# Performance work log

Hardware: AMD Instinct MI355X
Metric: run time of the kernel (lower is better)

## Reference

```python
import jax, jax.numpy as jnp
import numpy as np

# Static configuration (uniform ragged layout: every sequence has the same lengths)
B = 8          # number of sequences
QLEN = 256     # new query tokens per sequence
D = 1024       # embedding_dim
H = 16         # num_attention_heads
HD = D // H    # head dim = 64
FFN = 4096     # ffn_embedding_dim
PAGE = 16      # KV-cache page size
KV_TOTAL = 4096            # total KV length per sequence (prefix + new)
P = KV_TOTAL // PAGE       # pages per sequence = 256
NEW_PAGES = QLEN // PAGE   # pages occupied by the new tokens = 16
NUM_PAGES = B * P          # 2048
PREFIX = KV_TOTAL - QLEN   # cached prefix length per sequence
SCALE = HD ** -0.5
LN_EPS = 1e-5


def layer_norm(x, g, b):
    mu = jnp.mean(x, axis=-1, keepdims=True)
    var = jnp.mean(jnp.square(x - mu), axis=-1, keepdims=True)
    return (x - mu) * jax.lax.rsqrt(var + LN_EPS) * g + b


def setup_inputs() -> dict:
    key = jax.random.key(0)
    ks = jax.random.split(key, 12)
    s = 0.02
    inp = {
        "x": jax.random.normal(ks[0], (B * QLEN, D), jnp.float32),
        "pagetable": jax.random.normal(ks[1], (NUM_PAGES, 2, PAGE, H, HD), jnp.float32) * 0.5,
        "Wq": jax.random.normal(ks[2], (D, D), jnp.float32) * s,
        "bq": jnp.zeros((D,), jnp.float32),
        "Wk": jax.random.normal(ks[3], (D, D), jnp.float32) * s,
        "bk": jnp.zeros((D,), jnp.float32),
        "Wv": jax.random.normal(ks[4], (D, D), jnp.float32) * s,
        "bv": jnp.zeros((D,), jnp.float32),
        "Wo": jax.random.normal(ks[5], (D, D), jnp.float32) * s,
        "bo": jnp.zeros((D,), jnp.float32),
        "ln1_g": jnp.ones((D,), jnp.float32),
        "ln1_b": jnp.zeros((D,), jnp.float32),
        "W1": jax.random.normal(ks[6], (D, FFN), jnp.float32) * s,
        "b1": jnp.zeros((FFN,), jnp.float32),
        "W2": jax.random.normal(ks[7], (FFN, D), jnp.float32) * s,
        "b2": jnp.zeros((D,), jnp.float32),
        "lnf_g": jnp.ones((D,), jnp.float32),
        "lnf_b": jnp.zeros((D,), jnp.float32),
        "qo_indptr": jnp.arange(B + 1, dtype=jnp.int32) * QLEN,
        "paged_kv_indptr": jnp.arange(B + 1, dtype=jnp.int32) * P,
        "paged_kv_indices": jnp.arange(NUM_PAGES, dtype=jnp.int32),
        "paged_kv_last_page_len": jnp.full((B,), PAGE, jnp.int32),
        "layer_idx": 0,
    }
    return inp


def reference(x, pagetable, Wq, bq, Wk, bk, Wv, bv, Wo, bo,
              ln1_g, ln1_b, W1, b1, W2, b2, lnf_g, lnf_b,
              qo_indptr, paged_kv_indptr, paged_kv_indices,
              paged_kv_last_page_len, layer_idx):
    residual = x

    # ---- paged self-attention (post-LN path: layer_norm_first=False) ----
    q = ((x @ Wq + bq) * SCALE).reshape(B, QLEN, H, HD)
    k_new = (x @ Wk + bk).reshape(B, QLEN, H, HD)
    v_new = (x @ Wv + bv).reshape(B, QLEN, H, HD)

    # append new K/V into the last NEW_PAGES pages of each sequence
    page_ids = paged_kv_indices.reshape(B, P)                 # [B, P]
    new_ids = page_ids[:, P - NEW_PAGES:].reshape(-1)         # [B*NEW_PAGES]
    kv_new = jnp.stack([k_new, v_new], axis=2)                # [B, QLEN, 2, H, HD]
    kv_new = kv_new.reshape(B, NEW_PAGES, PAGE, 2, H, HD).transpose(0, 1, 3, 2, 4, 5)
    pt = pagetable.at[new_ids].set(kv_new.reshape(-1, 2, PAGE, H, HD))

    # gather the full paged KV per sequence
    kv = pt[page_ids]                                         # [B, P, 2, PAGE, H, HD]
    K = kv[:, :, 0].reshape(B, KV_TOTAL, H, HD)
    V = kv[:, :, 1].reshape(B, KV_TOTAL, H, HD)

    # streaming-causal mask: query i attends to kv positions <= PREFIX + i
    scores = jnp.einsum("bqhd,bkhd->bhqk", q, K)              # [B, H, QLEN, KV_TOTAL]
    kv_pos = jnp.arange(KV_TOTAL)[None, :]
    q_pos = PREFIX + jnp.arange(QLEN)[:, None]
    scores = jnp.where(kv_pos <= q_pos, scores, jnp.float32(-1e30))
    attn = jax.nn.softmax(scores, axis=-1)
    ctx = jnp.einsum("bhqk,bkhd->bqhd", attn, V).reshape(B * QLEN, D)
    x = ctx @ Wo + bo

    x = residual + x
    x = layer_norm(x, ln1_g, ln1_b)

    # ---- FFN ----
    residual = x
    x = jax.nn.relu(x @ W1 + b1)
    x = x @ W2 + b2
    layer_result = x
    x = residual + x
    x = layer_norm(x, lnf_g, lnf_b)

    return x, layer_result, pt
```

## Files before the change

kernel.cpp:

```cpp
#include <hip/hip_runtime.h>
#include <hip/hip_bf16.h>

typedef unsigned short u16;
typedef __attribute__((ext_vector_type(4))) float f32x4;
typedef __attribute__((ext_vector_type(8))) short short8;

#define MODE_QKV 0
#define MODE_WO  1
#define MODE_F1  2
#define MODE_F2  3

__device__ inline u16 f2bf(float f) {
    __hip_bfloat16 h = __float2bfloat16(f);
    return *(u16*)&h;
}
__device__ inline float bf2f(u16 u) {
    union { unsigned int i; float f; } x; x.i = ((unsigned int)u) << 16; return x.f;
}

typedef __attribute__((address_space(3))) unsigned int lds_u32_t;
typedef const __attribute__((address_space(1))) unsigned int glb_u32_t;
__device__ inline void gload16(const u16* g, u16* l) {
    __builtin_amdgcn_global_load_lds((glb_u32_t*)(const void*)g,
                                     (lds_u32_t*)(void*)l, 16, 0, 0);
}

__global__ __launch_bounds__(256) void prep_wx(
    const float* __restrict__ Wq, const float* __restrict__ Wk,
    const float* __restrict__ Wv, const float* __restrict__ x,
    u16* __restrict__ WqkvT, u16* __restrict__ xb) {
    int bid = blockIdx.x;
    int tid = threadIdx.x;
    int tx = tid & 31, ty = tid >> 5;
    if (bid >= 3072) {
        int i = (bid - 3072) * 256 + tid;
        const float4* p = (const float4*)(x + (size_t)i * 8);
        float4 a = p[0], b = p[1];
        u16 t[8] = {f2bf(a.x), f2bf(a.y), f2bf(a.z), f2bf(a.w),
                    f2bf(b.x), f2bf(b.y), f2bf(b.z), f2bf(b.w)};
        *(uint4*)(xb + (size_t)i * 8) = *(const uint4*)t;
        return;
    }
    int m = bid >> 10, r = bid & 1023;
    const float* src = (m == 0) ? Wq : (m == 1) ? Wk : Wv;
    u16* dst = WqkvT + (size_t)m * 1024 * 1024;
    __shared__ float t[32][33];
    int n0 = (r & 31) * 32, k0 = (r >> 5) * 32;
#pragma unroll
    for (int j = 0; j < 32; j += 8)
        t[ty + j][tx] = src[(size_t)(k0 + ty + j) * 1024 + n0 + tx];
    __syncthreads();
#pragma unroll
    for (int j = 0; j < 32; j += 8)
        dst[(size_t)(n0 + ty + j) * 1024 + k0 + tx] = f2bf(t[tx][ty + j]);
}

__global__ __launch_bounds__(256) void ln_wo(const float* __restrict__ p0,
                                             const float* __restrict__ p1,
                                             const float* __restrict__ bo,
                                             const float* __restrict__ resid,
                                             const float* __restrict__ g,
                                             const float* __restrict__ be,
                                             float* __restrict__ outf,
                                             u16* __restrict__ outb) {
    int row = blockIdx.x;
    int tid = threadIdx.x;
    int c = tid * 4;
    size_t o = (size_t)row * 1024 + c;
    f32x4 v = *(const f32x4*)(p0 + o) + *(const f32x4*)(p1 + o)
            + *(const f32x4*)(bo + c) + *(const f32x4*)(resid + o);
    float s = v[0] + v[1] + v[2] + v[3];
#pragma unroll
    for (int m = 1; m < 64; m <<= 1) s += __shfl_xor(s, m, 64);
    __shared__ float red1[4], red2[4];
    int w = tid >> 6;
    if ((tid & 63) == 0) red1[w] = s;
    __syncthreads();
    float mu = (red1[0] + red1[1] + red1[2] + red1[3]) * (1.0f / 1024.0f);
    f32x4 d = v - mu;
    float q = d[0] * d[0] + d[1] * d[1] + d[2] * d[2] + d[3] * d[3];
#pragma unroll
    for (int m = 1; m < 64; m <<= 1) q += __shfl_xor(q, m, 64);
    if ((tid & 63) == 0) red2[w] = q;
    __syncthreads();
    float var = (red2[0] + red2[1] + red2[2] + red2[3]) * (1.0f / 1024.0f);
    float rs = rsqrtf(var + 1e-5f);
    f32x4 gg = *(const f32x4*)(g + c), bb = *(const f32x4*)(be + c);
    f32x4 ov = d * rs * gg + bb;
    *(f32x4*)(outf + o) = ov;
    u16 t[4] = {f2bf(ov[0]), f2bf(ov[1]), f2bf(ov[2]), f2bf(ov[3])};
    *(uint2*)&outb[o] = *(const uint2*)t;
}

__global__ __launch_bounds__(256) void ln_f2(const float* __restrict__ q0,
                                             const float* __restrict__ b2,
                                             const float* __restrict__ xln1f,
                                             const float* __restrict__ g,
                                             const float* __restrict__ be,
                                             float* __restrict__ out_lr,
                                             float* __restrict__ out_x) {
    int row = blockIdx.x;
    int tid = threadIdx.x;
    int c = tid * 4;
    size_t o = (size_t)row * 1024 + c;
    const size_t st = (size_t)2048 * 1024;
    f32x4 v = *(const f32x4*)(q0 + o) + *(const f32x4*)(q0 + st + o)
            + *(const f32x4*)(q0 + 2 * st + o) + *(const f32x4*)(q0 + 3 * st + o)
            + *(const f32x4*)(b2 + c);
    *(f32x4*)(out_lr + o) = v;
    v = v + *(const f32x4*)(xln1f + o);
    float s = v[0] + v[1] + v[2] + v[3];
#pragma unroll
    for (int m = 1; m < 64; m <<= 1) s += __shfl_xor(s, m, 64);
    __shared__ float red1[4], red2[4];
    int w = tid >> 6;
    if ((tid & 63) == 0) red1[w] = s;
    __syncthreads();
    float mu = (red1[0] + red1[1] + red1[2] + red1[3]) * (1.0f / 1024.0f);
    f32x4 d = v - mu;
    float q = d[0] * d[0] + d[1] * d[1] + d[2] * d[2] + d[3] * d[3];
#pragma unroll
    for (int m = 1; m < 64; m <<= 1) q += __shfl_xor(q, m, 64);
    if ((tid & 63) == 0) red2[w] = q;
    __syncthreads();
    float var = (red2[0] + red2[1] + red2[2] + red2[3]) * (1.0f / 1024.0f);
    float rs = rsqrtf(var + 1e-5f);
    f32x4 gg = *(const f32x4*)(g + c), bb = *(const f32x4*)(be + c);
    *(f32x4*)(out_x + o) = d * rs * gg + bb;
}

template <int MODE>
__device__ __forceinline__ void gemm_body(
    u16* As, u16* Bs, int m0, int n0,
    const u16* __restrict__ A, const u16* __restrict__ Bt, int lda, int Kspan, int N,
    const float* __restrict__ bias0, const float* __restrict__ bias1,
    const float* __restrict__ bias2,
    float* __restrict__ o0, u16* __restrict__ ob,
    u16* __restrict__ kbf, u16* __restrict__ vbf, const int* __restrict__ kvidx) {
    int tid = threadIdx.x;
    int l = tid & 63, w = tid >> 6;
    int wr = w >> 1, wc = w & 1;
    int lr = l & 15, lg = l >> 4;
    int lrow8 = l >> 3;
    int scol = ((l & 7) ^ lrow8) << 3;
    f32x4 acc[4][4] = {};
    for (int kb = 0; kb < Kspan; kb += 64) {
#pragma unroll
        for (int p = 0; p < 4; ++p) {
            int chunk = p * 4 + w;
            int r = chunk * 8 + lrow8;
            gload16(&A[(size_t)(m0 + r) * lda + kb + scol], &As[chunk * 512]);
            gload16(&Bt[(size_t)(n0 + r) * lda + kb + scol], &Bs[chunk * 512]);
        }
        __syncthreads();
#pragma unroll
        for (int kk = 0; kk < 2; ++kk) {
            short8 a[4], b[4];
            int c0 = kk * 32 + lg * 8;
#pragma unroll
            for (int mi = 0; mi < 4; mi++) {
                int row = wr * 64 + mi * 16 + lr;
                a[mi] = *(const short8*)&As[row * 64 + (c0 ^ ((row & 7) << 3))];
            }
#pragma unroll
            for (int ni = 0; ni < 4; ni++) {
                int row = wc * 64 + ni * 16 + lr;
                b[ni] = *(const short8*)&Bs[row * 64 + (c0 ^ ((row & 7) << 3))];
            }
#pragma unroll
            for (int mi = 0; mi < 4; mi++)
#pragma unroll
                for (int ni = 0; ni < 4; ni++)
                    acc[mi][ni] = __builtin_amdgcn_mfma_f32_16x16x32_bf16(
                        a[mi], b[ni], acc[mi][ni], 0, 0, 0);
        }
        __syncthreads();
    }
#pragma unroll
    for (int mi = 0; mi < 4; mi++) {
#pragma unroll
        for (int ni = 0; ni < 4; ni++) {
#pragma unroll
            for (int r = 0; r < 4; r++) {
                int row = m0 + wr * 64 + mi * 16 + lg * 4 + r;
                int col = n0 + wc * 64 + ni * 16 + lr;
                float v = acc[mi][ni][r];
                if constexpr (MODE == MODE_QKV) {
                    int sel = col >> 10, c = col & 1023;
                    int b = row >> 8, ii = row & 255;
                    int h = (c >> 6), hd = c & 63;
                    if (sel == 0) {
                        ob[(size_t)row * 1024 + c] = f2bf((v + bias0[c]) * 0.125f);
                    } else if (sel == 1) {
                        float val = v + bias1[c];
                        int page = kvidx[b * 256 + 240 + (ii >> 4)];
                        o0[(size_t)page * 32768 + (size_t)(ii & 15) * 1024 + c] = val;
                        kbf[((size_t)(b * 16 + h) * 4096 + 3840 + ii) * 64 + hd] = f2bf(val);
                    } else {
                        float val = v + bias2[c];
                        int page = kvidx[b * 256 + 240 + (ii >> 4)];
                        o0[(size_t)page * 32768 + 16384 + (size_t)(ii & 15) * 1024 + c] = val;
                        vbf[((size_t)(b * 16 + h) * 64 + hd) * 4096 + 3840 + ii] = f2bf(val);
                    }
                } else if constexpr (MODE == MODE_F1) {
                    float t = v + bias0[col];
                    ob[(size_t)row * N + col] = f2bf(fmaxf(t, 0.0f));
                } else {
                    o0[(size_t)row * N + col] = v;
                }
            }
        }
    }
}

template <int MODE>
__global__ __launch_bounds__(256) void gemm_nt(
    const u16* __restrict__ A, const u16* __restrict__ Bt,
    int lda, int Kspan, int N, int gx, int nper,
    const float* __restrict__ bias0,
    float* __restrict__ o0, u16* __restrict__ ob, size_t osplit) {
    __shared__ __align__(16) u16 smem[128 * 64 * 2];
    int bid = blockIdx.x;
    int split = bid / nper, t = bid % nper;
    gemm_body<MODE>(smem, smem + 128 * 64, (t / gx) * 128, (t % gx) * 128,
                    A + (size_t)split * Kspan, Bt + (size_t)split * Kspan,
                    lda, Kspan, N, bias0, nullptr, nullptr,
                    o0 ? o0 + (size_t)split * osplit : nullptr, ob,
                    nullptr, nullptr, nullptr);
}

__global__ __launch_bounds__(256) void mega_prep(
    const u16* __restrict__ xb, const u16* __restrict__ WqkvT,
    const float* __restrict__ bq, const float* __restrict__ bk,
    const float* __restrict__ bv,
    float* __restrict__ out_pt, u16* __restrict__ qbuf,
    u16* __restrict__ Kbf, u16* __restrict__ Vtbf,
    const float* __restrict__ pgt, const int* __restrict__ kvidx) {
    __shared__ __align__(16) u16 smem[128 * 64 * 2];
    int bid = blockIdx.x;
    int tid = threadIdx.x;
    if (bid % 21 == 20) {
        int t = bid / 21;
        gemm_body<MODE_QKV>(smem, smem + 8192, (t / 24) * 128, (t % 24) * 128,
                            xb, WqkvT, 1024, 1024, 3072, bq, bk, bv,
                            out_pt, qbuf, Kbf, Vtbf, kvidx);
        return;
    }
    int idx = (bid / 21) * 20 + (bid % 21);
    int tile = idx % 60, rest = idx / 60;
    int h = rest & 15, b = rest >> 4;
    int T0 = tile * 64;
    int rr = tid >> 4;
    int hdq = tid & 15;
    u16* vt = smem;
    size_t kdst_base = ((size_t)(b * 16 + h) * 4096 + T0) * 64;
#pragma unroll
    for (int p = 0; p < 4; ++p) {
        int i = p * 16 + rr;
        int page = kvidx[b * 256 + (T0 >> 4) + p];
        size_t src = (size_t)page * 32768 + (size_t)rr * 1024 + h * 64 + hdq * 4;
        float4 kf = *(const float4*)(pgt + src);
        *(float4*)(out_pt + src) = kf;
        u16 kb4[4] = {f2bf(kf.x), f2bf(kf.y), f2bf(kf.z), f2bf(kf.w)};
        *(uint2*)&Kbf[kdst_base + (size_t)i * 64 + hdq * 4] = *(const uint2*)kb4;
        float4 vf = *(const float4*)(pgt + src + 16384);
        *(float4*)(out_pt + src + 16384) = vf;
        u16 vb4[4] = {f2bf(vf.x), f2bf(vf.y), f2bf(vf.z), f2bf(vf.w)};
        *(uint2*)&vt[i * 68 + hdq * 4] = *(const uint2*)vb4;
    }
    __syncthreads();
    size_t vdst_base = (size_t)(b * 16 + h) * 64 * 4096 + T0;
#pragma unroll
    for (int p = 0; p < 4; ++p) {
        int hd = p * 16 + rr;
        u16 o[4];
#pragma unroll
        for (int j = 0; j < 4; ++j) o[j] = vt[(hdq * 4 + j) * 68 + hd];
        *(uint2*)&Vtbf[vdst_base + (size_t)hd * 4096 + hdq * 4] = *(const uint2*)o;
    }
}

__global__ __launch_bounds__(512) void attn_kernel(const u16* __restrict__ qb,
                                                   const u16* __restrict__ Kbf,
                                                   const u16* __restrict__ Vtbf,
                                                   u16* __restrict__ pOct,
                                                   float* __restrict__ pL,
                                                   const float* __restrict__ Wo,
                                                   const float* __restrict__ W1,
                                                   const float* __restrict__ W2,
                                                   u16* __restrict__ WoT,
                                                   u16* __restrict__ W1T,
                                                   u16* __restrict__ W2T) {
    __shared__ u16 Ks[64 * 64];
    __shared__ u16 Vt[64 * 64];
    __shared__ u16 Ps[8][16 * 64];
    int bid = blockIdx.x;
    int tid = threadIdx.x;
    if (bid >= 1024) {
        int sub = tid >> 8, t2 = tid & 255;
        int wb = (bid - 1024) * 2 + sub;
        const float* src; u16* dst; int K, N, bx, by;
        if (wb < 1024) {
            bx = wb & 31; by = wb >> 5; K = 1024; N = 1024; src = Wo; dst = WoT;
        } else if (wb < 5120) {
            int r = wb - 1024; bx = r & 127; by = r >> 7; K = 1024; N = 4096; src = W1; dst = W1T;
        } else {
            int r = wb - 5120; bx = r & 31; by = r >> 5; K = 4096; N = 1024; src = W2; dst = W2T;
        }
        float* t = sub ? (float*)Vt : (float*)Ks;
        int tx = t2 & 31, ty = t2 >> 5;
        int n0 = bx * 32, k0 = by * 32;
#pragma unroll
        for (int jj = 0; jj < 32; jj += 8)
            t[(ty + jj) * 33 + tx] = src[(size_t)(k0 + ty + jj) * N + n0 + tx];
        __syncthreads();
#pragma unroll
        for (int jj = 0; jj < 32; jj += 8)
            dst[(size_t)(n0 + ty + jj) * K + k0 + tx] = f2bf(t[tx * 33 + ty + jj]);
        return;
    }
    int l = tid & 63, w = tid >> 6;
    int lr = l & 15, lg = l >> 4;
    int x = bid & 7, qt = x >> 2, split = x & 3;
    int h = (bid >> 3) & 15, b = bid >> 7;

    int qrow = qt * 128 + w * 16 + lr;
    const u16* qptr = qb + (size_t)(b * 256 + qrow) * 1024 + h * 64 + lg * 8;
    short8 qf0 = *(const short8*)qptr;
    short8 qf1 = *(const short8*)(qptr + 32);

    const u16* kslab = Kbf + (size_t)(b * 16 + h) * 4096 * 64;
    const u16* vslab = Vtbf + (size_t)(b * 16 + h) * 64 * 4096;

    f32x4 octx[4] = {};
    f32x4 lacc = {};
    short8 ones;
#pragma unroll
    for (int jj = 0; jj < 8; jj++) ones[jj] = (short)0x3F80;

    int qbase = 3840 + qt * 128;
    int ntiles = (qbase + 128) >> 6;
    int tstart = split * 16;
    int tend = min(tstart + 16, ntiles);
    int kt0 = tstart * 64, kt1 = tend * 64;

    int srow = tid >> 3, scol8 = (tid & 7) * 8;
    int sdst = srow * 64 + (scol8 ^ ((srow & 7) << 3));
    const u16* kp = kslab + srow * 64 + scol8;
    const u16* vp = vslab + (size_t)srow * 4096 + scol8;

    uint4 kreg = *(const uint4*)(kp + (size_t)kt0 * 64);
    uint4 vreg = *(const uint4*)(vp + kt0);
    for (int kt = kt0; kt < kt1; kt += 64) {
        *(uint4*)&Ks[sdst] = kreg;
        *(uint4*)&Vt[sdst] = vreg;
        __syncthreads();
        bool hn = (kt + 64) < kt1;
        if (hn) {
            kreg = *(const uint4*)(kp + (size_t)(kt + 64) * 64);
            vreg = *(const uint4*)(vp + kt + 64);
        }
        float P[4][4];
        bool need_mask = (kt + 63 > qbase);
        __builtin_amdgcn_s_setprio(1);
#pragma unroll
        for (int ni = 0; ni < 4; ni++) {
            f32x4 s = {};
            int krow = ni * 16 + lr;
            int swz = (krow & 7) << 3;
            short8 k0 = *(const short8*)&Ks[krow * 64 + ((lg * 8) ^ swz)];
            short8 k1 = *(const short8*)&Ks[krow * 64 + ((32 + lg * 8) ^ swz)];
            s = __builtin_amdgcn_mfma_f32_16x16x32_bf16(qf0, k0, s, 0, 0, 0);
            s = __builtin_amdgcn_mfma_f32_16x16x32_bf16(qf1, k1, s, 0, 0, 0);
            if (need_mask) {
                int col = kt + ni * 16 + lr;
#pragma unroll
                for (int r = 0; r < 4; r++) {
                    int q = qt * 128 + w * 16 + lg * 4 + r;
                    P[ni][r] = (col <= 3840 + q) ? __expf(s[r]) : 0.0f;
                }
            } else {
#pragma unroll
                for (int r = 0; r < 4; r++) P[ni][r] = __expf(s[r]);
            }
        }
        __builtin_amdgcn_s_setprio(0);
#pragma unroll
        for (int ni = 0; ni < 4; ni++)
#pragma unroll
            for (int r = 0; r < 4; r++) {
                int prow = lg * 4 + r;
                Ps[w][prow * 64 + ((ni * 16 + lr) ^ ((prow & 7) << 3))] = f2bf(P[ni][r]);
            }
        __builtin_amdgcn_s_setprio(1);
#pragma unroll
        for (int kk = 0; kk < 2; kk++) {
            int c0 = kk * 32 + lg * 8;
            short8 pf = *(const short8*)&Ps[w][lr * 64 + (c0 ^ ((lr & 7) << 3))];
            lacc = __builtin_amdgcn_mfma_f32_16x16x32_bf16(pf, ones, lacc, 0, 0, 0);
#pragma unroll
            for (int dt = 0; dt < 4; dt++) {
                int vrow = dt * 16 + lr;
                short8 vf = *(const short8*)&Vt[vrow * 64 + (c0 ^ ((vrow & 7) << 3))];
                octx[dt] = __builtin_amdgcn_mfma_f32_16x16x32_bf16(pf, vf, octx[dt], 0, 0, 0);
            }
        }
        __builtin_amdgcn_s_setprio(0);
        __syncthreads();
    }
    size_t obase = (((size_t)(split * 8 + b) * 16 + h) * 256 + qt * 128) * 64;
#pragma unroll
    for (int dt = 0; dt < 4; dt++)
#pragma unroll
        for (int r = 0; r < 4; r++)
            pOct[obase + (size_t)(w * 16 + lg * 4 + r) * 64 + dt * 16 + lr] =
                f2bf(octx[dt][r]);
    if (lr == 0) {
        size_t lbase = ((size_t)(split * 8 + b) * 16 + h) * 256 + qt * 128;
#pragma unroll
        for (int r = 0; r < 4; r++) pL[lbase + w * 16 + lg * 4 + r] = lacc[r];
    }
}

__global__ __launch_bounds__(256) void attn_combine(const u16* __restrict__ pOct,
                                                    const float* __restrict__ pL,
                                                    u16* __restrict__ ctxb) {
    int row = blockIdx.x;
    int b = row >> 8, q = row & 255;
    int tid = threadIdx.x;
    int h = tid >> 4, dq = (tid & 15) * 4;
    size_t stride = (size_t)128 * 256 * 64;
    size_t base = ((size_t)(b * 16 + h) * 256 + q) * 64 + dq;
    size_t lstride = 128 * 256;
    size_t lbase = (size_t)(b * 16 + h) * 256 + q;
    f32x4 s = {};
    float ls = 0.0f;
#pragma unroll
    for (int sp = 0; sp < 4; sp++) {
        u16 a[4];
        *(uint2*)a = *(const uint2*)&pOct[sp * stride + base];
#pragma unroll
        for (int j = 0; j < 4; j++) s[j] += bf2f(a[j]);
        ls += pL[sp * lstride + lbase];
    }
    float inv = 1.0f / ls;
    u16 o[4] = {f2bf(s[0] * inv), f2bf(s[1] * inv), f2bf(s[2] * inv), f2bf(s[3] * inv)};
    *(uint2*)&ctxb[(size_t)row * 1024 + h * 64 + dq] = *(const uint2*)o;
}

extern "C" void kernel_launch(void* const* d_in, const int* in_sizes, int n_in,
                              void* d_out, int out_size, void* d_ws, size_t ws_size,
                              hipStream_t stream) {
    (void)in_sizes; (void)n_in; (void)out_size; (void)ws_size;
    const float* x   = (const float*)d_in[0];
    const float* pgt = (const float*)d_in[1];
    const float* Wq  = (const float*)d_in[2];
    const float* bq  = (const float*)d_in[3];
    const float* Wk  = (const float*)d_in[4];
    const float* bk  = (const float*)d_in[5];
    const float* Wv  = (const float*)d_in[6];
    const float* bv  = (const float*)d_in[7];
    const float* Wo  = (const float*)d_in[8];
    const float* bo  = (const float*)d_in[9];
    const float* ln1g = (const float*)d_in[10];
    const float* ln1b = (const float*)d_in[11];
    const float* W1  = (const float*)d_in[12];
    const float* b1  = (const float*)d_in[13];
    const float* W2  = (const float*)d_in[14];
    const float* b2  = (const float*)d_in[15];
    const float* lnfg = (const float*)d_in[16];
    const float* lnfb = (const float*)d_in[17];
    const int* kvidx = (const int*)d_in[20];

    float* out = (float*)d_out;
    float* out_x  = out;
    float* out_lr = out + 2048 * 1024;
    float* out_pt = out + 2 * 2048 * 1024;

    char* ws = (char*)d_ws;
    size_t off = 0;
    auto alloc = [&](size_t bytes) { void* p = ws + off; off += (bytes + 255) & ~(size_t)255; return p; };
    u16* WqkvT = (u16*)alloc((size_t)3072 * 1024 * 2);
    u16* WoT   = (u16*)alloc((size_t)1024 * 1024 * 2);
    u16* W1T   = (u16*)alloc((size_t)4096 * 1024 * 2);
    u16* W2T   = (u16*)alloc((size_t)1024 * 4096 * 2);
    u16* xb    = (u16*)alloc((size_t)2048 * 1024 * 2);
    u16* qbuf  = (u16*)alloc((size_t)2048 * 1024 * 2);
    u16* ctxb  = (u16*)alloc((size_t)2048 * 1024 * 2);
    char* regB = (char*)alloc((size_t)168 * 1024 * 1024);
    u16* Kbf  = (u16*)regB;
    u16* Vtbf = (u16*)(regB + (size_t)64 * 1024 * 1024);
    u16*   pOct = (u16*)(regB + (size_t)128 * 1024 * 1024);
    float* pL   = (float*)(regB + (size_t)162 * 1024 * 1024);
    float* p0    = (float*)regB;
    float* xln1f = (float*)(regB + (size_t)16 * 1024 * 1024);
    u16*   xln1b = (u16*)(regB + (size_t)24 * 1024 * 1024);
    u16*   hb    = (u16*)(regB + (size_t)32 * 1024 * 1024);
    float* q0    = (float*)(regB + (size_t)128 * 1024 * 1024);

    prep_wx<<<4096, 256, 0, stream>>>(Wq, Wk, Wv, x, WqkvT, xb);
    mega_prep<<<8064, 256, 0, stream>>>(xb, WqkvT, bq, bk, bv,
                                        out_pt, qbuf, Kbf, Vtbf, pgt, kvidx);
    attn_kernel<<<5632, 512, 0, stream>>>(qbuf, Kbf, Vtbf, pOct, pL,
                                          Wo, W1, W2, WoT, W1T, W2T);
    attn_combine<<<2048, 256, 0, stream>>>(pOct, pL, ctxb);
    gemm_nt<MODE_WO><<<256, 256, 0, stream>>>(ctxb, WoT, 1024, 512, 1024, 8, 128,
        nullptr, p0, nullptr, (size_t)2048 * 1024);
    ln_wo<<<2048, 256, 0, stream>>>(p0, p0 + (size_t)2048 * 1024, bo, x,
                                    ln1g, ln1b, xln1f, xln1b);
    gemm_nt<MODE_F1><<<512, 256, 0, stream>>>(xln1b, W1T, 1024, 1024, 4096, 32, 512,
        b1, nullptr, hb, 0);
    gemm_nt<MODE_F2><<<512, 256, 0, stream>>>(hb, W2T, 4096, 1024, 1024, 8, 128,
        nullptr, q0, nullptr, (size_t)2048 * 1024);
    ln_f2<<<2048, 256, 0, stream>>>(q0, b2, xln1f, lnfg, lnfb, out_lr, out_x);
}
```

Baseline: 328.0 us.

## Fuse split-KV attention combine into Wo GEMM A-tile load and remap attention blocks

Removes the separate attn_combine kernel and ctx buffer. The new gemm_wo kernel reduces the four split partial outputs and normalizes by the summed denominators while building each A tile in LDS, then runs the MFMA GEMM against WoT. This saves a launch and a round trip of the bf16 context through global memory, but each A-tile load now does synchronous scalar loads and arithmetic with no async overlap. The attention kernel's block-index mapping is also reordered so consecutive blocks spread across different (batch, head) groups, which may change cache locality and load balance.

```diff
diff --git a/kernel.cpp b/kernel.cpp
--- a/kernel.cpp
+++ b/kernel.cpp
@@ -229,6 +229,85 @@
                     nullptr, nullptr, nullptr);
 }
 
+__global__ __launch_bounds__(256) void gemm_wo(
+    const u16* __restrict__ pOct, const float* __restrict__ pL,
+    const u16* __restrict__ Bt, float* __restrict__ p0) {
+    __shared__ __align__(16) u16 As[128 * 64];
+    __shared__ __align__(16) u16 Bs[128 * 64];
+    int bid = blockIdx.x;
+    int split = bid >> 7, t = bid & 127;
+    int m0 = (t >> 3) * 128, n0 = (t & 7) * 128;
+    int tid = threadIdx.x;
+    int l = tid & 63, w = tid >> 6;
+    int wr = w >> 1, wc = w & 1;
+    int lr = l & 15, lg = l >> 4;
+    int lrow8 = l >> 3;
+    int scol = ((l & 7) ^ lrow8) << 3;
+    int acol = (l & 7) << 3;
+    int bb = m0 >> 8, q0 = m0 & 255;
+    f32x4 acc[4][4] = {};
+    for (int kb = 0; kb < 512; kb += 64) {
+        int k0 = split * 512 + kb;
+        int h = k0 >> 6;
+#pragma unroll
+        for (int p = 0; p < 4; ++p) {
+            int chunk = p * 4 + w;
+            int r = chunk * 8 + lrow8;
+            size_t rowbase = ((size_t)bb * 16 + h) * 256 + q0 + r;
+            gload16(&Bt[(size_t)(n0 + r) * 1024 + k0 + scol], &Bs[chunk * 512]);
+            float ls = pL[rowbase] + pL[32768 + rowbase]
+                     + pL[2 * 32768 + rowbase] + pL[3 * 32768 + rowbase];
+            float inv = 1.0f / ls;
+            float sums[8] = {};
+#pragma unroll
+            for (int sp = 0; sp < 4; ++sp) {
+                u16 a8[8];
+                *(uint4*)a8 = *(const uint4*)&pOct[((size_t)sp * 32768 + rowbase) * 64 + acol];
+#pragma unroll
+                for (int j = 0; j < 8; ++j) sums[j] += bf2f(a8[j]);
+            }
+            u16 o8[8];
+#pragma unroll
+            for (int j = 0; j < 8; ++j) o8[j] = f2bf(sums[j] * inv);
+            *(uint4*)&As[(size_t)r * 64 + (acol ^ ((r & 7) << 3))] = *(const uint4*)o8;
+        }
+        __syncthreads();
+#pragma unroll
+        for (int kk = 0; kk < 2; ++kk) {
+            short8 a[4], b[4];
+            int c0 = kk * 32 + lg * 8;
+#pragma unroll
+            for (int mi = 0; mi < 4; mi++) {
+                int row = wr * 64 + mi * 16 + lr;
+                a[mi] = *(const short8*)&As[row * 64 + (c0 ^ ((row & 7) << 3))];
+            }
+#pragma unroll
+            for (int ni = 0; ni < 4; ni++) {
+                int row = wc * 64 + ni * 16 + lr;
+                b[ni] = *(const short8*)&Bs[row * 64 + (c0 ^ ((row & 7) << 3))];
+            }
+#pragma unroll
+            for (int mi = 0; mi < 4; mi++)
+#pragma unroll
+                for (int ni = 0; ni < 4; ni++)
+                    acc[mi][ni] = __builtin_amdgcn_mfma_f32_16x16x32_bf16(
+                        a[mi], b[ni], acc[mi][ni], 0, 0, 0);
+        }
+        __syncthreads();
+    }
+    float* o0 = p0 + (size_t)split * 2048 * 1024;
+#pragma unroll
+    for (int mi = 0; mi < 4; mi++)
+#pragma unroll
+        for (int ni = 0; ni < 4; ni++)
+#pragma unroll
+            for (int r = 0; r < 4; r++) {
+                int row = m0 + wr * 64 + mi * 16 + lg * 4 + r;
+                int col = n0 + wc * 64 + ni * 16 + lr;
+                o0[(size_t)row * 1024 + col] = acc[mi][ni][r];
+            }
+}
+
 __global__ __launch_bounds__(256) void mega_prep(
     const u16* __restrict__ xb, const u16* __restrict__ WqkvT,
     const float* __restrict__ bq, const float* __restrict__ bk,
@@ -319,10 +398,13 @@
             dst[(size_t)(n0 + ty + jj) * K + k0 + tx] = f2bf(t[tx * 33 + ty + jj]);
         return;
     }
+    int xg = bid & 7, tt = bid >> 3;
+    int j = tt & 7, ghi = tt >> 3;
+    int g = (ghi << 3) | xg;
+    int b = g >> 4, h = g & 15;
+    int qt = j >> 2, split = j & 3;
     int l = tid & 63, w = tid >> 6;
     int lr = l & 15, lg = l >> 4;
-    int x = bid & 7, qt = x >> 2, split = x & 3;
-    int h = (bid >> 3) & 15, b = bid >> 7;
 
     int qrow = qt * 128 + w * 16 + lr;
     const u16* qptr = qb + (size_t)(b * 256 + qrow) * 1024 + h * 64 + lg * 8;
@@ -420,32 +502,6 @@
 #pragma unroll
         for (int r = 0; r < 4; r++) pL[lbase + w * 16 + lg * 4 + r] = lacc[r];
     }
-}
-
-__global__ __launch_bounds__(256) void attn_combine(const u16* __restrict__ pOct,
-                                                    const float* __restrict__ pL,
-                                                    u16* __restrict__ ctxb) {
-    int row = blockIdx.x;
-    int b = row >> 8, q = row & 255;
-    int tid = threadIdx.x;
-    int h = tid >> 4, dq = (tid & 15) * 4;
-    size_t stride = (size_t)128 * 256 * 64;
-    size_t base = ((size_t)(b * 16 + h) * 256 + q) * 64 + dq;
-    size_t lstride = 128 * 256;
-    size_t lbase = (size_t)(b * 16 + h) * 256 + q;
-    f32x4 s = {};
-    float ls = 0.0f;
-#pragma unroll
-    for (int sp = 0; sp < 4; sp++) {
-        u16 a[4];
-        *(uint2*)a = *(const uint2*)&pOct[sp * stride + base];
-#pragma unroll
-        for (int j = 0; j < 4; j++) s[j] += bf2f(a[j]);
-        ls += pL[sp * lstride + lbase];
-    }
-    float inv = 1.0f / ls;
-    u16 o[4] = {f2bf(s[0] * inv), f2bf(s[1] * inv), f2bf(s[2] * inv), f2bf(s[3] * inv)};
-    *(uint2*)&ctxb[(size_t)row * 1024 + h * 64 + dq] = *(const uint2*)o;
 }
 
 extern "C" void kernel_launch(void* const* d_in, const int* in_sizes, int n_in,
@@ -486,7 +542,6 @@
     u16* W2T   = (u16*)alloc((size_t)1024 * 4096 * 2);
     u16* xb    = (u16*)alloc((size_t)2048 * 1024 * 2);
     u16* qbuf  = (u16*)alloc((size_t)2048 * 1024 * 2);
-    u16* ctxb  = (u16*)alloc((size_t)2048 * 1024 * 2);
     char* regB = (char*)alloc((size_t)168 * 1024 * 1024);
     u16* Kbf  = (u16*)regB;
     u16* Vtbf = (u16*)(regB + (size_t)64 * 1024 * 1024);
@@ -503,9 +558,7 @@
                                         out_pt, qbuf, Kbf, Vtbf, pgt, kvidx);
     attn_kernel<<<5632, 512, 0, stream>>>(qbuf, Kbf, Vtbf, pOct, pL,
                                           Wo, W1, W2, WoT, W1T, W2T);
-    attn_combine<<<2048, 256, 0, stream>>>(pOct, pL, ctxb);
-    gemm_nt<MODE_WO><<<256, 256, 0, stream>>>(ctxb, WoT, 1024, 512, 1024, 8, 128,
-        nullptr, p0, nullptr, (size_t)2048 * 1024);
+    gemm_wo<<<256, 256, 0, stream>>>(pOct, pL, WoT, p0);
     ln_wo<<<2048, 256, 0, stream>>>(p0, p0 + (size_t)2048 * 1024, bo, x,
                                     ln1g, ln1b, xln1f, xln1b);
     gemm_nt<MODE_F1><<<512, 256, 0, stream>>>(xln1b, W1T, 1024, 1024, 4096, 32, 512,
```

Measured after the change: 368.7 us. 12.4% more time.
